# Kernel optimization log

Hardware: AMD Instinct MI355X
Metric: run time of the kernel (lower is better)

Reference implementation:

```python
import jax, jax.numpy as jnp
import numpy as np

B, R, S = 4, 16384, 96

def setup_inputs() -> dict:
    key = jax.random.key(0)
    k1, k2, k3, k4 = jax.random.split(key, 4)
    colors = jax.random.normal(k1, (B, R, S, 3), dtype=jnp.float32)
    densities = jax.random.normal(k2, (B, R, S, 1), dtype=jnp.float32)
    # depths must be monotonically increasing along the sample axis
    depths = jnp.sort(jax.random.uniform(k3, (B, R, S, 1), dtype=jnp.float32), axis=2)
    sample_coordinates = jax.random.uniform(k4, (B, R, S, 3), dtype=jnp.float32)
    return {"colors": colors, "densities": densities, "depths": depths,
            "sample_coordinates": sample_coordinates, "white_back": 0}


def reference(colors, densities, depths, sample_coordinates, white_back):
    deltas = depths[:, :, 1:] - depths[:, :, :-1]                     # [B,R,S-1,1]
    colors_mid = (colors[:, :, :-1] + colors[:, :, 1:]) * 0.5
    densities_mid = (densities[:, :, :-1] + densities[:, :, 1:]) * 0.5
    depths_mid = (depths[:, :, :-1] + depths[:, :, 1:]) * 0.5
    coords_mid = (sample_coordinates[:, :, :-1] + sample_coordinates[:, :, 1:]) * 0.5

    densities_mid = jax.nn.softplus(densities_mid)                    # activation_factory
    alpha = 1.0 - jnp.exp(-densities_mid * deltas)                    # [B,R,S-1,1]

    ones = jnp.ones_like(alpha[:, :, :1])
    alpha_shifted = jnp.concatenate([ones, 1.0 - alpha + 1e-10], axis=-2)
    trans = jnp.cumprod(alpha_shifted, axis=-2)[:, :, :-1]            # transmittance T_i

    weights = alpha * trans                                            # [B,R,S-1,1]
    tau = trans[:, :, -1, :]                                           # [B,R,1]

    composite_rgb = jnp.sum(weights * colors_mid, axis=-2)             # [B,R,3]
    composite_point = jnp.sum(weights * coords_mid, axis=-2)           # [B,R,3]
    weight_total = jnp.sum(weights, axis=2)                            # [B,R,1]

    composite_depth = jnp.sum(weights * depths_mid, axis=-2)           # [B,R,1]
    composite_depth = jnp.nan_to_num(composite_depth, nan=jnp.inf)
    composite_depth = jnp.clip(composite_depth, jnp.min(depths), jnp.max(depths))

    composite_rgb = jnp.where(white_back != 0,
                              composite_rgb + 1.0 - weight_total,
                              composite_rgb)
    return composite_rgb, composite_depth, weights, composite_point, tau
```

## Files before the change

### kernel.cpp

```cpp
#include <hip/hip_runtime.h>

#define NRAYS 65536
#define NS    96
#define NI    95

#define OFF_RGB   0
#define OFF_DEPTH 196608
#define OFF_W     262144
#define OFF_PT    6488064
#define OFF_TAU   6684672

__global__ void depth_minmax_sorted(const float* __restrict__ deps, unsigned* ws) {
    const int t = blockIdx.x * blockDim.x + threadIdx.x;
    float lo = deps[(size_t)t * NS];
    float hi = deps[(size_t)t * NS + (NS - 1)];
    #pragma unroll
    for (int off = 32; off; off >>= 1) {
        lo = fminf(lo, __shfl_xor(lo, off, 64));
        hi = fmaxf(hi, __shfl_xor(hi, off, 64));
    }
    if ((threadIdx.x & 63) == 0) {
        atomicMin(&ws[0], __float_as_uint(lo));
        atomicMin(&ws[1], ~__float_as_uint(hi));
    }
}

__device__ __forceinline__ float softplus_fast(float x) {
    return fmaxf(x, 0.0f) + __logf(1.0f + __expf(-fabsf(x)));
}

__launch_bounds__(256)
__global__ void raymarch(const float* __restrict__ colors,
                         const float* __restrict__ dens,
                         const float* __restrict__ deps,
                         const float* __restrict__ coords,
                         const int* __restrict__ wbp,
                         const unsigned* __restrict__ mm,
                         float* __restrict__ out) {
    const int lane = threadIdx.x & 63;
    const int sub  = lane & 15;
    const int g    = blockIdx.x * 16 + (threadIdx.x >> 4);

    float d[6], n[6], c[18], p[18];
    {
        const float2* q = (const float2*)(deps + (size_t)g * NS) + 3 * sub;
        #pragma unroll
        for (int j = 0; j < 3; ++j) { float2 v = q[j]; d[2*j] = v.x; d[2*j+1] = v.y; }
    }
    {
        const float2* q = (const float2*)(dens + (size_t)g * NS) + 3 * sub;
        #pragma unroll
        for (int j = 0; j < 3; ++j) { float2 v = q[j]; n[2*j] = v.x; n[2*j+1] = v.y; }
    }
    {
        const float2* q = (const float2*)(colors + (size_t)g * NS * 3) + 9 * sub;
        #pragma unroll
        for (int j = 0; j < 9; ++j) { float2 v = q[j]; c[2*j] = v.x; c[2*j+1] = v.y; }
    }
    {
        const float2* q = (const float2*)(coords + (size_t)g * NS * 3) + 9 * sub;
        #pragma unroll
        for (int j = 0; j < 9; ++j) { float2 v = q[j]; p[2*j] = v.x; p[2*j+1] = v.y; }
    }

    const int nsrc = (lane & 48) | ((sub + 1) & 15);
    float d6  = __shfl(d[0], nsrc, 64);
    float n6  = __shfl(n[0], nsrc, 64);
    float cn0 = __shfl(c[0], nsrc, 64);
    float cn1 = __shfl(c[1], nsrc, 64);
    float cn2 = __shfl(c[2], nsrc, 64);
    float pn0 = __shfl(p[0], nsrc, 64);
    float pn1 = __shfl(p[1], nsrc, 64);
    float pn2 = __shfl(p[2], nsrc, 64);

    float a[6], f[6];
    #pragma unroll
    for (int i = 0; i < 6; ++i) {
        float dn1 = (i < 5) ? d[i+1] : d6;
        float nn1 = (i < 5) ? n[i+1] : n6;
        float E = __expf(-softplus_fast(0.5f * (n[i] + nn1)) * (dn1 - d[i]));
        const bool valid = (i < 5) || (sub < 15);
        a[i] = valid ? (1.0f - E) : 0.0f;
        f[i] = valid ? (E + 1e-10f) : 1.0f;
    }

    float incl = ((f[0] * f[1]) * (f[2] * f[3])) * (f[4] * f[5]);
    #pragma unroll
    for (int off = 1; off < 16; off <<= 1) {
        float t = __shfl_up(incl, off, 16);
        if (sub >= off) incl *= t;
    }
    float excl = __shfl_up(incl, 1, 16);
    if (sub == 0) excl = 1.0f;

    float acc[8];
    #pragma unroll
    for (int k = 0; k < 8; ++k) acc[k] = 0.0f;
    float t = excl;
    float tauc = 0.0f;
    const size_t wb = (size_t)OFF_W + (size_t)g * NI + 6 * sub;
    #pragma unroll
    for (int i = 0; i < 6; ++i) {
        float w = a[i] * t;
        if (i < 5 || sub < 15) out[wb + i] = w;
        float dn1 = (i < 5) ? d[i+1] : d6;
        float dm  = 0.5f * (d[i] + dn1);
        float cmx = 0.5f * (c[3*i+0] + ((i < 5) ? c[3*i+3] : cn0));
        float cmy = 0.5f * (c[3*i+1] + ((i < 5) ? c[3*i+4] : cn1));
        float cmz = 0.5f * (c[3*i+2] + ((i < 5) ? c[3*i+5] : cn2));
        float pmx = 0.5f * (p[3*i+0] + ((i < 5) ? p[3*i+3] : pn0));
        float pmy = 0.5f * (p[3*i+1] + ((i < 5) ? p[3*i+4] : pn1));
        float pmz = 0.5f * (p[3*i+2] + ((i < 5) ? p[3*i+5] : pn2));
        acc[0] += w * cmx;  acc[1] += w * cmy;  acc[2] += w * cmz;
        acc[3] += w * pmx;  acc[4] += w * pmy;  acc[5] += w * pmz;
        acc[6] += w * dm;   acc[7] += w;
        if (i == 4) tauc = t;
        t *= f[i];
    }
    float tau = __shfl(tauc, (lane & 48) | 15, 64);

    #pragma unroll
    for (int k = 0; k < 8; ++k) {
        #pragma unroll
        for (int off = 1; off < 16; off <<= 1)
            acc[k] += __shfl_xor(acc[k], off, 64);
    }

    if (sub == 0) {
        float add = (wbp != nullptr && wbp[0] != 0) ? (1.0f - acc[7]) : 0.0f;
        size_t rb = (size_t)OFF_RGB + (size_t)g * 3;
        out[rb + 0] = acc[0] + add;
        out[rb + 1] = acc[1] + add;
        out[rb + 2] = acc[2] + add;
        size_t pb = (size_t)OFF_PT + (size_t)g * 3;
        out[pb + 0] = acc[3];
        out[pb + 1] = acc[4];
        out[pb + 2] = acc[5];
        float cd = acc[6];
        if (cd != cd) cd = __int_as_float(0x7f800000);
        float dmin = __uint_as_float(mm[0]);
        float dmax = __uint_as_float(~mm[1]);
        cd = fminf(fmaxf(cd, dmin), dmax);
        out[OFF_DEPTH + g] = cd;
        out[OFF_TAU + g]   = tau;
    }
}

extern "C" void kernel_launch(void* const* d_in, const int* in_sizes, int n_in,
                              void* d_out, int out_size, void* d_ws, size_t ws_size,
                              hipStream_t stream) {
    const float* colors = (const float*)d_in[0];
    const float* dens   = (const float*)d_in[1];
    const float* deps   = (const float*)d_in[2];
    const float* coords = (const float*)d_in[3];
    const int*   wb     = (n_in > 4) ? (const int*)d_in[4] : nullptr;
    float* out = (float*)d_out;
    unsigned* mm = (unsigned*)d_ws;

    hipMemsetAsync(mm, 0xFF, 8, stream);
    depth_minmax_sorted<<<NRAYS / 256, 256, 0, stream>>>(deps, mm);
    raymarch<<<NRAYS / 16, 256, 0, stream>>>(colors, dens, deps, coords, wb, mm, out);
}
```

Baseline: 236.2 us.

## Stage ray inputs through per-wave LDS with coalesced vector loads

Each wave now loads the contiguous data for its four rays with lane-contiguous float2/float4 global loads. It then transposes that data through a per-wave shared-memory buffer into the per-thread sample layout, and takes each segment's neighbour values from LDS instead of wave shuffles. The aim is to replace the strided per-thread float2 loads, which fetch 72-byte-strided chunks, with fully coalesced transactions. The buffer is reused for colors and then coords. The kernel also gets a minimum-occupancy launch bound, which may constrain register allocation, and it relies on in-order LDS access within a wave since there is no explicit barrier.

```diff
diff --git a/kernel.cpp b/kernel.cpp
--- a/kernel.cpp
+++ b/kernel.cpp
@@ -29,7 +29,7 @@
     return fmaxf(x, 0.0f) + __logf(1.0f + __expf(-fabsf(x)));
 }
 
-__launch_bounds__(256)
+__launch_bounds__(256, 5)
 __global__ void raymarch(const float* __restrict__ colors,
                          const float* __restrict__ dens,
                          const float* __restrict__ deps,
@@ -37,41 +37,83 @@
                          const int* __restrict__ wbp,
                          const unsigned* __restrict__ mm,
                          float* __restrict__ out) {
-    const int lane = threadIdx.x & 63;
+    __shared__ float sbuf[4 * 1152];
+
+    const int tid  = threadIdx.x;
+    const int lane = tid & 63;
+    const int wv   = tid >> 6;
     const int sub  = lane & 15;
-    const int g    = blockIdx.x * 16 + (threadIdx.x >> 4);
-
-    float d[6], n[6], c[18], p[18];
-    {
-        const float2* q = (const float2*)(deps + (size_t)g * NS) + 3 * sub;
-        #pragma unroll
-        for (int j = 0; j < 3; ++j) { float2 v = q[j]; d[2*j] = v.x; d[2*j+1] = v.y; }
-    }
-    {
-        const float2* q = (const float2*)(dens + (size_t)g * NS) + 3 * sub;
-        #pragma unroll
-        for (int j = 0; j < 3; ++j) { float2 v = q[j]; n[2*j] = v.x; n[2*j+1] = v.y; }
-    }
-    {
-        const float2* q = (const float2*)(colors + (size_t)g * NS * 3) + 9 * sub;
+    const int r4   = lane >> 4;
+    const int g    = blockIdx.x * 16 + wv * 4 + r4;
+
+    const size_t rb0 = (size_t)blockIdx.x * 16 + wv * 4;
+    const float2* dg2 = (const float2*)(deps + rb0 * NS);
+    const float2* ng2 = (const float2*)(dens + rb0 * NS);
+    float2 dr[3], nr[3];
+    #pragma unroll
+    for (int k = 0; k < 3; ++k) dr[k] = dg2[lane + 64 * k];
+    #pragma unroll
+    for (int k = 0; k < 3; ++k) nr[k] = ng2[lane + 64 * k];
+    const float4* cg4 = (const float4*)(colors + rb0 * NS * 3);
+    const float4* pg4 = (const float4*)(coords + rb0 * NS * 3);
+    float4 cr[4], pr[4];
+    #pragma unroll
+    for (int k = 0; k < 4; ++k) cr[k] = cg4[lane + 64 * k];
+    float2 crt = ((const float2*)(colors + rb0 * NS * 3 + 1024))[lane];
+    #pragma unroll
+    for (int k = 0; k < 4; ++k) pr[k] = pg4[lane + 64 * k];
+    float2 prt = ((const float2*)(coords + rb0 * NS * 3 + 1024))[lane];
+
+    float* wreg = sbuf + wv * 1152;
+
+    {
+        float2* s2 = (float2*)wreg;
+        #pragma unroll
+        for (int k = 0; k < 3; ++k) s2[lane + 64 * k] = dr[k];
+        #pragma unroll
+        for (int k = 0; k < 3; ++k) s2[192 + lane + 64 * k] = nr[k];
+    }
+    float d[6], n[6], d6, n6;
+    {
+        const float2* qd = (const float2*)(wreg + r4 * 96 + 6 * sub);
+        const float2* qn = (const float2*)(wreg + 384 + r4 * 96 + 6 * sub);
+        #pragma unroll
+        for (int j = 0; j < 3; ++j) { float2 v = qd[j]; d[2*j] = v.x; d[2*j+1] = v.y; }
+        #pragma unroll
+        for (int j = 0; j < 3; ++j) { float2 v = qn[j]; n[2*j] = v.x; n[2*j+1] = v.y; }
+        const int noff = (sub < 15) ? 6 * (sub + 1) : 0;
+        d6 = wreg[r4 * 96 + noff];
+        n6 = wreg[384 + r4 * 96 + noff];
+    }
+
+    float4* s4 = (float4*)wreg;
+    #pragma unroll
+    for (int k = 0; k < 4; ++k) s4[lane + 64 * k] = cr[k];
+    ((float2*)wreg)[512 + lane] = crt;
+    float c[18], cn0, cn1, cn2;
+    {
+        const float2* q = (const float2*)(wreg + r4 * 288 + 18 * sub);
         #pragma unroll
         for (int j = 0; j < 9; ++j) { float2 v = q[j]; c[2*j] = v.x; c[2*j+1] = v.y; }
-    }
-    {
-        const float2* q = (const float2*)(coords + (size_t)g * NS * 3) + 9 * sub;
+        const int noff = (sub < 15) ? 18 * (sub + 1) : 0;
+        cn0 = wreg[r4 * 288 + noff + 0];
+        cn1 = wreg[r4 * 288 + noff + 1];
+        cn2 = wreg[r4 * 288 + noff + 2];
+    }
+
+    #pragma unroll
+    for (int k = 0; k < 4; ++k) s4[lane + 64 * k] = pr[k];
+    ((float2*)wreg)[512 + lane] = prt;
+    float p[18], pn0, pn1, pn2;
+    {
+        const float2* q = (const float2*)(wreg + r4 * 288 + 18 * sub);
         #pragma unroll
         for (int j = 0; j < 9; ++j) { float2 v = q[j]; p[2*j] = v.x; p[2*j+1] = v.y; }
-    }
-
-    const int nsrc = (lane & 48) | ((sub + 1) & 15);
-    float d6  = __shfl(d[0], nsrc, 64);
-    float n6  = __shfl(n[0], nsrc, 64);
-    float cn0 = __shfl(c[0], nsrc, 64);
-    float cn1 = __shfl(c[1], nsrc, 64);
-    float cn2 = __shfl(c[2], nsrc, 64);
-    float pn0 = __shfl(p[0], nsrc, 64);
-    float pn1 = __shfl(p[1], nsrc, 64);
-    float pn2 = __shfl(p[2], nsrc, 64);
+        const int noff = (sub < 15) ? 18 * (sub + 1) : 0;
+        pn0 = wreg[r4 * 288 + noff + 0];
+        pn1 = wreg[r4 * 288 + noff + 1];
+        pn2 = wreg[r4 * 288 + noff + 2];
+    }
 
     float a[6], f[6];
     #pragma unroll
```

Measured after the change: 238.5 us. Within noise of the previous version (+1.0%).

## Stage colors and coords through LDS via async global_load_lds

Applied to the files above, without the earlier changes.

Colors and sample coordinates are now copied per wave into shared memory with the global_load_lds builtin in fully coalesced 16-byte chunks. Depths and densities are still loaded straight into registers, and the transmittance scan runs while the async copies are in flight. Neighbour values are then read from LDS instead of shuffled across lanes. The aim is to replace strided 8-byte global loads with contiguous wide transfers and overlap memory latency with compute, at the cost of LDS use, a manual vmcnt wait and a new occupancy hint (launch_bounds 256,4).

```diff
diff --git a/kernel.cpp b/kernel.cpp
--- a/kernel.cpp
+++ b/kernel.cpp
@@ -29,7 +29,14 @@
     return fmaxf(x, 0.0f) + __logf(1.0f + __expf(-fabsf(x)));
 }
 
-__launch_bounds__(256)
+__device__ __forceinline__ void gload_lds16(const float* gp, float* lp) {
+    __builtin_amdgcn_global_load_lds(
+        (const __attribute__((address_space(1))) void*)gp,
+        (__attribute__((address_space(3))) void*)lp,
+        16, 0, 0);
+}
+
+__launch_bounds__(256, 4)
 __global__ void raymarch(const float* __restrict__ colors,
                          const float* __restrict__ dens,
                          const float* __restrict__ deps,
@@ -37,41 +44,44 @@
                          const int* __restrict__ wbp,
                          const unsigned* __restrict__ mm,
                          float* __restrict__ out) {
-    const int lane = threadIdx.x & 63;
+    __shared__ float sbuf[4 * 2304];
+
+    const int tid  = threadIdx.x;
+    const int lane = tid & 63;
+    const int wv   = tid >> 6;
     const int sub  = lane & 15;
-    const int g    = blockIdx.x * 16 + (threadIdx.x >> 4);
+    const int r4   = lane >> 4;
+    const int g    = blockIdx.x * 16 + wv * 4 + r4;
+    const size_t rb0 = (size_t)blockIdx.x * 16 + wv * 4;
 
-    float d[6], n[6], c[18], p[18];
+    const float2* dq = (const float2*)(deps + (size_t)g * NS + 6 * sub);
+    const float2* nq = (const float2*)(dens + (size_t)g * NS + 6 * sub);
+    float2 dv0 = dq[0], dv1 = dq[1], dv2 = dq[2];
+    float2 nv0 = nq[0], nv1 = nq[1], nv2 = nq[2];
+
+    __builtin_amdgcn_sched_barrier(0);
+
+    float* cl = sbuf + wv * 2304;
+    float* pl = cl + 1152;
     {
-        const float2* q = (const float2*)(deps + (size_t)g * NS) + 3 * sub;
+        const float* cg = colors + rb0 * (NS * 3);
+        const float* pg = coords + rb0 * (NS * 3);
         #pragma unroll
-        for (int j = 0; j < 3; ++j) { float2 v = q[j]; d[2*j] = v.x; d[2*j+1] = v.y; }
-    }
-    {
-        const float2* q = (const float2*)(dens + (size_t)g * NS) + 3 * sub;
+        for (int k = 0; k < 4; ++k) gload_lds16(cg + 4 * lane + 256 * k, cl + 256 * k);
         #pragma unroll
-        for (int j = 0; j < 3; ++j) { float2 v = q[j]; n[2*j] = v.x; n[2*j+1] = v.y; }
-    }
-    {
-        const float2* q = (const float2*)(colors + (size_t)g * NS * 3) + 9 * sub;
-        #pragma unroll
-        for (int j = 0; j < 9; ++j) { float2 v = q[j]; c[2*j] = v.x; c[2*j+1] = v.y; }
-    }
-    {
-        const float2* q = (const float2*)(coords + (size_t)g * NS * 3) + 9 * sub;
-        #pragma unroll
-        for (int j = 0; j < 9; ++j) { float2 v = q[j]; p[2*j] = v.x; p[2*j+1] = v.y; }
+        for (int k = 0; k < 4; ++k) gload_lds16(pg + 4 * lane + 256 * k, pl + 256 * k);
+        if (lane < 32) {
+            gload_lds16(cg + 1024 + 4 * lane, cl + 1024);
+            gload_lds16(pg + 1024 + 4 * lane, pl + 1024);
+        }
     }
 
+    float d[6], n[6];
+    d[0] = dv0.x; d[1] = dv0.y; d[2] = dv1.x; d[3] = dv1.y; d[4] = dv2.x; d[5] = dv2.y;
+    n[0] = nv0.x; n[1] = nv0.y; n[2] = nv1.x; n[3] = nv1.y; n[4] = nv2.x; n[5] = nv2.y;
     const int nsrc = (lane & 48) | ((sub + 1) & 15);
-    float d6  = __shfl(d[0], nsrc, 64);
-    float n6  = __shfl(n[0], nsrc, 64);
-    float cn0 = __shfl(c[0], nsrc, 64);
-    float cn1 = __shfl(c[1], nsrc, 64);
-    float cn2 = __shfl(c[2], nsrc, 64);
-    float pn0 = __shfl(p[0], nsrc, 64);
-    float pn1 = __shfl(p[1], nsrc, 64);
-    float pn2 = __shfl(p[2], nsrc, 64);
+    float d6 = __shfl(d[0], nsrc, 64);
+    float n6 = __shfl(n[0], nsrc, 64);
 
     float a[6], f[6];
     #pragma unroll
@@ -92,6 +102,25 @@
     }
     float excl = __shfl_up(incl, 1, 16);
     if (sub == 0) excl = 1.0f;
+
+    asm volatile("s_waitcnt vmcnt(0)" ::: "memory");
+
+    float c[18], p[18], cn0, cn1, cn2, pn0, pn1, pn2;
+    {
+        const float2* qc = (const float2*)(cl + r4 * 288 + 18 * sub);
+        const float2* qp = (const float2*)(pl + r4 * 288 + 18 * sub);
+        #pragma unroll
+        for (int j = 0; j < 9; ++j) { float2 v = qc[j]; c[2*j] = v.x; c[2*j+1] = v.y; }
+        #pragma unroll
+        for (int j = 0; j < 9; ++j) { float2 v = qp[j]; p[2*j] = v.x; p[2*j+1] = v.y; }
+        const int noff = (sub < 15) ? 18 * (sub + 1) : 0;
+        cn0 = cl[r4 * 288 + noff + 0];
+        cn1 = cl[r4 * 288 + noff + 1];
+        cn2 = cl[r4 * 288 + noff + 2];
+        pn0 = pl[r4 * 288 + noff + 0];
+        pn1 = pl[r4 * 288 + noff + 1];
+        pn2 = pl[r4 * 288 + noff + 2];
+    }
 
     float acc[8];
     #pragma unroll
```

Result: no change. 236.9 us (+0.3%).

## Stream ray inputs through double-buffered LDS via async global_load_lds in persistent waves

Applied to the files above, without the earlier changes.

Replaces the one-shot register loads with a persistent single-wave block that processes 16 ray pairs. Each pair's inputs are fetched by asynchronous global_load_lds into a double-buffered LDS ring, with vmcnt waits so the next pair's load overlaps current compute. It also remaps blocks across groups and splits each ray over 32 lanes instead of 16. The aim is better memory-level parallelism and coalesced 16-byte loads. The risks are lower occupancy from 64-thread blocks, hand-tuned waitcnt correctness, and the lack of an LDS barrier or wait between the global_load_lds writes and the reads, which depends on in-order completion.

```diff
diff --git a/kernel.cpp b/kernel.cpp
--- a/kernel.cpp
+++ b/kernel.cpp
@@ -29,7 +29,38 @@
     return fmaxf(x, 0.0f) + __logf(1.0f + __expf(-fabsf(x)));
 }
 
-__launch_bounds__(256)
+__device__ __forceinline__ void gload_lds16(const float* gp, float* lp) {
+    __builtin_amdgcn_global_load_lds(
+        (const __attribute__((address_space(1))) void*)gp,
+        (__attribute__((address_space(3))) void*)lp,
+        16, 0, 0);
+}
+
+__device__ __forceinline__ void issue_dma2(const float* __restrict__ colors,
+                                           const float* __restrict__ coords,
+                                           const float* __restrict__ deps,
+                                           const float* __restrict__ dens,
+                                           int grp, float* lbuf, int lane) {
+    const size_t rb0 = (size_t)grp * 2;
+    const float* cg = colors + rb0 * (NS * 3);
+    const float* pg = coords + rb0 * (NS * 3);
+    const float* dg = deps   + rb0 * NS;
+    const float* ng = dens   + rb0 * NS;
+    gload_lds16(cg +       4 * lane, lbuf);
+    gload_lds16(cg + 256 + 4 * lane, lbuf + 256);
+    gload_lds16(pg +       4 * lane, lbuf + 576);
+    gload_lds16(pg + 256 + 4 * lane, lbuf + 832);
+    if (lane < 48) {
+        gload_lds16(dg + 4 * lane, lbuf + 1152);
+        gload_lds16(ng + 4 * lane, lbuf + 1344);
+    }
+    if (lane < 16) {
+        gload_lds16(cg + 512 + 4 * lane, lbuf + 512);
+        gload_lds16(pg + 512 + 4 * lane, lbuf + 1088);
+    }
+}
+
+__launch_bounds__(64)
 __global__ void raymarch(const float* __restrict__ colors,
                          const float* __restrict__ dens,
                          const float* __restrict__ deps,
@@ -37,112 +68,125 @@
                          const int* __restrict__ wbp,
                          const unsigned* __restrict__ mm,
                          float* __restrict__ out) {
-    const int lane = threadIdx.x & 63;
-    const int sub  = lane & 15;
-    const int g    = blockIdx.x * 16 + (threadIdx.x >> 4);
-
-    float d[6], n[6], c[18], p[18];
-    {
-        const float2* q = (const float2*)(deps + (size_t)g * NS) + 3 * sub;
-        #pragma unroll
-        for (int j = 0; j < 3; ++j) { float2 v = q[j]; d[2*j] = v.x; d[2*j+1] = v.y; }
-    }
-    {
-        const float2* q = (const float2*)(dens + (size_t)g * NS) + 3 * sub;
-        #pragma unroll
-        for (int j = 0; j < 3; ++j) { float2 v = q[j]; n[2*j] = v.x; n[2*j+1] = v.y; }
-    }
-    {
-        const float2* q = (const float2*)(colors + (size_t)g * NS * 3) + 9 * sub;
-        #pragma unroll
-        for (int j = 0; j < 9; ++j) { float2 v = q[j]; c[2*j] = v.x; c[2*j+1] = v.y; }
-    }
-    {
-        const float2* q = (const float2*)(coords + (size_t)g * NS * 3) + 9 * sub;
-        #pragma unroll
-        for (int j = 0; j < 9; ++j) { float2 v = q[j]; p[2*j] = v.x; p[2*j+1] = v.y; }
-    }
-
-    const int nsrc = (lane & 48) | ((sub + 1) & 15);
-    float d6  = __shfl(d[0], nsrc, 64);
-    float n6  = __shfl(n[0], nsrc, 64);
-    float cn0 = __shfl(c[0], nsrc, 64);
-    float cn1 = __shfl(c[1], nsrc, 64);
-    float cn2 = __shfl(c[2], nsrc, 64);
-    float pn0 = __shfl(p[0], nsrc, 64);
-    float pn1 = __shfl(p[1], nsrc, 64);
-    float pn2 = __shfl(p[2], nsrc, 64);
-
-    float a[6], f[6];
-    #pragma unroll
-    for (int i = 0; i < 6; ++i) {
-        float dn1 = (i < 5) ? d[i+1] : d6;
-        float nn1 = (i < 5) ? n[i+1] : n6;
-        float E = __expf(-softplus_fast(0.5f * (n[i] + nn1)) * (dn1 - d[i]));
-        const bool valid = (i < 5) || (sub < 15);
-        a[i] = valid ? (1.0f - E) : 0.0f;
-        f[i] = valid ? (E + 1e-10f) : 1.0f;
-    }
-
-    float incl = ((f[0] * f[1]) * (f[2] * f[3])) * (f[4] * f[5]);
-    #pragma unroll
-    for (int off = 1; off < 16; off <<= 1) {
-        float t = __shfl_up(incl, off, 16);
-        if (sub >= off) incl *= t;
-    }
-    float excl = __shfl_up(incl, 1, 16);
-    if (sub == 0) excl = 1.0f;
-
-    float acc[8];
-    #pragma unroll
-    for (int k = 0; k < 8; ++k) acc[k] = 0.0f;
-    float t = excl;
-    float tauc = 0.0f;
-    const size_t wb = (size_t)OFF_W + (size_t)g * NI + 6 * sub;
-    #pragma unroll
-    for (int i = 0; i < 6; ++i) {
-        float w = a[i] * t;
-        if (i < 5 || sub < 15) out[wb + i] = w;
-        float dn1 = (i < 5) ? d[i+1] : d6;
-        float dm  = 0.5f * (d[i] + dn1);
-        float cmx = 0.5f * (c[3*i+0] + ((i < 5) ? c[3*i+3] : cn0));
-        float cmy = 0.5f * (c[3*i+1] + ((i < 5) ? c[3*i+4] : cn1));
-        float cmz = 0.5f * (c[3*i+2] + ((i < 5) ? c[3*i+5] : cn2));
-        float pmx = 0.5f * (p[3*i+0] + ((i < 5) ? p[3*i+3] : pn0));
-        float pmy = 0.5f * (p[3*i+1] + ((i < 5) ? p[3*i+4] : pn1));
-        float pmz = 0.5f * (p[3*i+2] + ((i < 5) ? p[3*i+5] : pn2));
-        acc[0] += w * cmx;  acc[1] += w * cmy;  acc[2] += w * cmz;
-        acc[3] += w * pmx;  acc[4] += w * pmy;  acc[5] += w * pmz;
-        acc[6] += w * dm;   acc[7] += w;
-        if (i == 4) tauc = t;
-        t *= f[i];
-    }
-    float tau = __shfl(tauc, (lane & 48) | 15, 64);
-
-    #pragma unroll
-    for (int k = 0; k < 8; ++k) {
-        #pragma unroll
-        for (int off = 1; off < 16; off <<= 1)
-            acc[k] += __shfl_xor(acc[k], off, 64);
-    }
-
-    if (sub == 0) {
-        float add = (wbp != nullptr && wbp[0] != 0) ? (1.0f - acc[7]) : 0.0f;
-        size_t rb = (size_t)OFF_RGB + (size_t)g * 3;
-        out[rb + 0] = acc[0] + add;
-        out[rb + 1] = acc[1] + add;
-        out[rb + 2] = acc[2] + add;
-        size_t pb = (size_t)OFF_PT + (size_t)g * 3;
-        out[pb + 0] = acc[3];
-        out[pb + 1] = acc[4];
-        out[pb + 2] = acc[5];
-        float cd = acc[6];
-        if (cd != cd) cd = __int_as_float(0x7f800000);
-        float dmin = __uint_as_float(mm[0]);
-        float dmax = __uint_as_float(~mm[1]);
-        cd = fminf(fmaxf(cd, dmin), dmax);
-        out[OFF_DEPTH + g] = cd;
-        out[OFF_TAU + g]   = tau;
+    __shared__ float sbuf[2 * 1536];
+
+    const int lane = threadIdx.x;
+    const int sub  = lane & 31;
+    const int r2   = lane >> 5;
+
+    const int blk = (blockIdx.x & 7) * 256 + (blockIdx.x >> 3);
+
+    issue_dma2(colors, coords, deps, dens, blk * 16 + 0, sbuf,        lane);
+    issue_dma2(colors, coords, deps, dens, blk * 16 + 1, sbuf + 1536, lane);
+
+    for (int it = 0; it < 16; ++it) {
+        float* lb = sbuf + (it & 1) * 1536;
+
+        if (it < 15) asm volatile("s_waitcnt vmcnt(8)" ::: "memory");
+        else         asm volatile("s_waitcnt vmcnt(0)" ::: "memory");
+        __builtin_amdgcn_sched_barrier(0);
+
+        const int grp = blk * 16 + it;
+        const int g   = grp * 2 + r2;
+
+        float d[3], n[3], c[9], p[9];
+        {
+            const int db = 1152 + r2 * 96 + 3 * sub;
+            const int nb = 1344 + r2 * 96 + 3 * sub;
+            #pragma unroll
+            for (int j = 0; j < 3; ++j) { d[j] = lb[db + j]; n[j] = lb[nb + j]; }
+            const int cb = r2 * 288 + 9 * sub;
+            const int pb = 576 + r2 * 288 + 9 * sub;
+            #pragma unroll
+            for (int j = 0; j < 9; ++j) { c[j] = lb[cb + j]; p[j] = lb[pb + j]; }
+        }
+        const int no3 = (sub < 31) ? 3 * (sub + 1) : 0;
+        const int no9 = (sub < 31) ? 9 * (sub + 1) : 0;
+        float d3  = lb[1152 + r2 * 96 + no3];
+        float n3  = lb[1344 + r2 * 96 + no3];
+        float cn0 = lb[r2 * 288 + no9 + 0];
+        float cn1 = lb[r2 * 288 + no9 + 1];
+        float cn2 = lb[r2 * 288 + no9 + 2];
+        float pn0 = lb[576 + r2 * 288 + no9 + 0];
+        float pn1 = lb[576 + r2 * 288 + no9 + 1];
+        float pn2 = lb[576 + r2 * 288 + no9 + 2];
+
+        float a[3], f[3];
+        #pragma unroll
+        for (int j = 0; j < 3; ++j) {
+            float dn1 = (j < 2) ? d[j+1] : d3;
+            float nn1 = (j < 2) ? n[j+1] : n3;
+            float E = __expf(-softplus_fast(0.5f * (n[j] + nn1)) * (dn1 - d[j]));
+            const bool valid = (j < 2) || (sub < 31);
+            a[j] = valid ? (1.0f - E) : 0.0f;
+            f[j] = valid ? (E + 1e-10f) : 1.0f;
+        }
+
+        float incl = f[0] * f[1] * f[2];
+        #pragma unroll
+        for (int off = 1; off < 32; off <<= 1) {
+            float t = __shfl_up(incl, off, 32);
+            if (sub >= off) incl *= t;
+        }
+        float excl = __shfl_up(incl, 1, 32);
+        if (sub == 0) excl = 1.0f;
+
+        float acc[8];
+        #pragma unroll
+        for (int k = 0; k < 8; ++k) acc[k] = 0.0f;
+        float t = excl;
+        float tauc = 0.0f;
+        const size_t wb = (size_t)OFF_W + (size_t)g * NI + 3 * sub;
+        #pragma unroll
+        for (int j = 0; j < 3; ++j) {
+            float w = a[j] * t;
+            if (j < 2 || sub < 31) out[wb + j] = w;
+            float dn1 = (j < 2) ? d[j+1] : d3;
+            float dm  = 0.5f * (d[j] + dn1);
+            float cmx = 0.5f * (c[3*j+0] + ((j < 2) ? c[3*j+3] : cn0));
+            float cmy = 0.5f * (c[3*j+1] + ((j < 2) ? c[3*j+4] : cn1));
+            float cmz = 0.5f * (c[3*j+2] + ((j < 2) ? c[3*j+5] : cn2));
+            float pmx = 0.5f * (p[3*j+0] + ((j < 2) ? p[3*j+3] : pn0));
+            float pmy = 0.5f * (p[3*j+1] + ((j < 2) ? p[3*j+4] : pn1));
+            float pmz = 0.5f * (p[3*j+2] + ((j < 2) ? p[3*j+5] : pn2));
+            acc[0] += w * cmx;  acc[1] += w * cmy;  acc[2] += w * cmz;
+            acc[3] += w * pmx;  acc[4] += w * pmy;  acc[5] += w * pmz;
+            acc[6] += w * dm;   acc[7] += w;
+            if (j == 1) tauc = t;
+            t *= f[j];
+        }
+        float tau = __shfl(tauc, (lane & 32) | 31, 64);
+
+        #pragma unroll
+        for (int k = 0; k < 8; ++k) {
+            #pragma unroll
+            for (int off = 1; off < 32; off <<= 1)
+                acc[k] += __shfl_xor(acc[k], off, 64);
+        }
+
+        if (sub == 0) {
+            float add = (wbp != nullptr && wbp[0] != 0) ? (1.0f - acc[7]) : 0.0f;
+            size_t rb = (size_t)OFF_RGB + (size_t)g * 3;
+            out[rb + 0] = acc[0] + add;
+            out[rb + 1] = acc[1] + add;
+            out[rb + 2] = acc[2] + add;
+            size_t pb = (size_t)OFF_PT + (size_t)g * 3;
+            out[pb + 0] = acc[3];
+            out[pb + 1] = acc[4];
+            out[pb + 2] = acc[5];
+            float cd = acc[6];
+            if (cd != cd) cd = __int_as_float(0x7f800000);
+            float dmin = __uint_as_float(mm[0]);
+            float dmax = __uint_as_float(~mm[1]);
+            cd = fminf(fmaxf(cd, dmin), dmax);
+            out[OFF_DEPTH + g] = cd;
+            out[OFF_TAU + g]   = tau;
+        }
+
+        if (it < 14) {
+            __builtin_amdgcn_sched_barrier(0);
+            issue_dma2(colors, coords, deps, dens, blk * 16 + it + 2, lb, lane);
+        }
     }
 }
 
@@ -159,5 +203,5 @@
 
     hipMemsetAsync(mm, 0xFF, 8, stream);
     depth_minmax_sorted<<<NRAYS / 256, 256, 0, stream>>>(deps, mm);
-    raymarch<<<NRAYS / 16, 256, 0, stream>>>(colors, dens, deps, coords, wb, mm, out);
-}
+    raymarch<<<2048, 64, 0, stream>>>(colors, dens, deps, coords, wb, mm, out);
+}
```

New measurement: 249.1 us. +5.5%, slower.
